# Optimization experiments

Hardware: AMD Instinct MI355X
Metric: run time of the kernel (lower is better)

Reference implementation:

```python
import jax, jax.numpy as jnp
import numpy as np

M, N = 4096, 4096


def _makhoul_perm(n):
    # Makhoul even/odd reordering: v[k] = x[2k] for k < ceil(n/2),
    # v[n-1-k] = x[2k+1] for the rest. This is the same input permutation
    # the dct2_fft2 kernel applies before its rfft2.
    idx = np.empty(n, dtype=np.int32)
    half = (n + 1) // 2
    idx[:half] = 2 * np.arange(half)
    idx[half:] = 2 * (n - 1 - np.arange(half, n)) + 1
    return jnp.asarray(idx)


def _dct2_1d_last(x):
    # Unnormalized DCT-II along the last axis via a same-length FFT plus
    # twiddle (expk) multiply:  C[k] = Re( exp(-i*pi*k/(2n)) * FFT(v)[k] )
    # which equals sum_m x[m] * cos(pi*k*(2m+1)/(2n)).
    n = x.shape[-1]
    v = jnp.take(x, _makhoul_perm(n), axis=-1)
    V = jnp.fft.fft(v, axis=-1)
    k = jnp.arange(n)
    expk = jnp.exp((-1j * np.pi / (2.0 * n)) * k)  # twiddle factors (expkM/expkN)
    return jnp.real(V * expk).astype(x.dtype)


def setup_inputs() -> dict:
    key = jax.random.key(0)
    x = jax.random.normal(key, (M, N), dtype=jnp.float32)
    return {"x": x}


def reference(x):
    # Separable 2D DCT-II: along axis -1 (uses expkN), then axis -2 (expkM).
    y = _dct2_1d_last(x)        # DCT over columns index (length N)
    y = _dct2_1d_last(y.T).T    # DCT over rows index (length M)
    return y
```

## Files before the change

### kernel.cpp

```cpp
#include <hip/hip_runtime.h>
#include <stdint.h>


#define NF 4096

__device__ __forceinline__ int physi(int e) { return e ^ ((e >> 4) & 15); }

__device__ __forceinline__ float2 cadd(float2 a, float2 b) {
    float2 r; r.x = a.x + b.x; r.y = a.y + b.y; return r;
}
__device__ __forceinline__ float2 csub(float2 a, float2 b) {
    float2 r; r.x = a.x - b.x; r.y = a.y - b.y; return r;
}
__device__ __forceinline__ float2 cmulc(float2 a, float2 b) {
    float2 r; r.x = a.x * b.x - a.y * b.y; r.y = a.x * b.y + a.y * b.x; return r;
}
__device__ __forceinline__ float2 rotm(float2 a) {
    float2 r; r.x = a.y; r.y = -a.x; return r;
}

__global__ __launch_bounds__(256) void setup_tables(float* __restrict__ tw,
                                                    float* __restrict__ ek) {
    int idx = blockIdx.x * 256 + threadIdx.x;
    if (idx < 4672) {
        int Ls, rel;
        if (idx < 64)       { Ls = 8;   rel = idx; }
        else if (idx < 576) { Ls = 64;  rel = idx - 64; }
        else                { Ls = 512; rel = idx - 576; }
        int p = rel >> 3, u = rel & 7;
        float phi = (float)(p * u) * (6.283185307179586f / (8.0f * (float)Ls));
        float s, c; __sincosf(phi, &s, &c);
        tw[2 * idx]     = c;
        tw[2 * idx + 1] = -s;
    } else if (idx < 8768) {
        int k = idx - 4672;
        float th = (float)k * (3.141592653589793f / 8192.0f);
        float s, c; __sincosf(th, &s, &c);
        ek[2 * k]     = c;
        ek[2 * k + 1] = s;
    }
}

#define RADIX8(x, E0, E1, E2, E3, O0, g1, g2, g3)                              \
    float2 t0 = cadd(x[0], x[4]), t1 = csub(x[0], x[4]);                       \
    float2 t2 = cadd(x[2], x[6]), t3 = csub(x[2], x[6]);                       \
    float2 E0 = cadd(t0, t2), E2 = csub(t0, t2);                               \
    float2 r3 = rotm(t3);                                                      \
    float2 E1 = cadd(t1, r3), E3 = csub(t1, r3);                               \
    float2 s0 = cadd(x[1], x[5]), s1 = csub(x[1], x[5]);                       \
    float2 s2 = cadd(x[3], x[7]), s3 = csub(x[3], x[7]);                       \
    float2 O0 = cadd(s0, s2), O2 = csub(s0, s2);                               \
    float2 r7 = rotm(s3);                                                      \
    float2 O1 = cadd(s1, r7), O3 = csub(s1, r7);                               \
    const float SQ = 0.7071067811865476f;                                      \
    float2 g1; g1.x = SQ * (O1.x + O1.y); g1.y = SQ * (O1.y - O1.x);           \
    float2 g2 = rotm(O2);                                                      \
    float2 g3; g3.x = SQ * (O3.y - O3.x); g3.y = -SQ * (O3.x + O3.y);

__global__ __launch_bounds__(512) void dct_rows(const float* __restrict__ In,
                                                float* __restrict__ Out,
                                                const float* __restrict__ tw,
                                                const float* __restrict__ ek) {
    __shared__ float2 buf[NF];
    const int j = threadIdx.x;
    const int b = blockIdx.x;
    const float* in0 = In + (size_t)(2 * b) * NF;
    const float* in1 = in0 + NF;
    float* out0 = Out + (size_t)b * NF;
    float* out1 = Out + (size_t)(4095 - b) * NF;

    float2 x[8];

    #pragma unroll
    for (int k = 0; k < 8; ++k) {
        int n = j + 512 * k;
        int idx = (n < 2048) ? (2 * n) : (8191 - 2 * n);
        x[k].x = in0[idx];
        x[k].y = in1[idx];
    }
    {
        RADIX8(x, E0, E1, E2, E3, O0, g1, g2, g3)
        int wb = 8 * j;
        buf[physi(wb)]     = cadd(E0, O0);
        buf[physi(wb + 1)] = cadd(E1, g1);
        buf[physi(wb + 2)] = cadd(E2, g2);
        buf[physi(wb + 3)] = cadd(E3, g3);
        buf[physi(wb + 4)] = csub(E0, O0);
        buf[physi(wb + 5)] = csub(E1, g1);
        buf[physi(wb + 6)] = csub(E2, g2);
        buf[physi(wb + 7)] = csub(E3, g3);
    }
    __syncthreads();

    #pragma unroll
    for (int t = 1; t < 3; ++t) {
        const int Ls = 1 << (3 * t);
        const int twoff = (t == 1) ? 0 : 64;
        const int p = j & (Ls - 1);
        const int q = j >> (3 * t);
        #pragma unroll
        for (int k = 0; k < 8; ++k)
            x[k] = buf[physi(j + 512 * k)];
        const float2* twp = (const float2*)tw + twoff + p * 8;
        #pragma unroll
        for (int k = 1; k < 8; ++k)
            x[k] = cmulc(x[k], twp[k]);
        RADIX8(x, E0, E1, E2, E3, O0, g1, g2, g3)
        __syncthreads();
        int wb = p + 8 * Ls * q;
        buf[physi(wb)]          = cadd(E0, O0);
        buf[physi(wb + Ls)]     = cadd(E1, g1);
        buf[physi(wb + 2 * Ls)] = cadd(E2, g2);
        buf[physi(wb + 3 * Ls)] = cadd(E3, g3);
        buf[physi(wb + 4 * Ls)] = csub(E0, O0);
        buf[physi(wb + 5 * Ls)] = csub(E1, g1);
        buf[physi(wb + 6 * Ls)] = csub(E2, g2);
        buf[physi(wb + 7 * Ls)] = csub(E3, g3);
        __syncthreads();
    }

    float2 o[8];
    {
        #pragma unroll
        for (int k = 0; k < 8; ++k)
            x[k] = buf[physi(j + 512 * k)];
        const float2* twp = (const float2*)tw + 576 + j * 8;
        #pragma unroll
        for (int k = 1; k < 8; ++k)
            x[k] = cmulc(x[k], twp[k]);
        RADIX8(x, E0, E1, E2, E3, O0, g1, g2, g3)
        o[0] = cadd(E0, O0); o[1] = cadd(E1, g1);
        o[2] = cadd(E2, g2); o[3] = cadd(E3, g3);
        o[4] = csub(E0, O0); o[5] = csub(E1, g1);
        o[6] = csub(E2, g2); o[7] = csub(E3, g3);
        #pragma unroll
        for (int r = 0; r < 8; ++r)
            buf[physi(j + 512 * r)] = o[r];
    }
    __syncthreads();

    #pragma unroll
    for (int i = 0; i < 8; ++i) {
        int k = j + 512 * i;
        int m = (NF - k) & (NF - 1);
        float2 Zk = o[i];
        float2 Zm = buf[physi(m)];
        float2 E = ((const float2*)ek)[k];
        out0[k] = 0.5f * ((Zk.x + Zm.x) * E.x + (Zk.y - Zm.y) * E.y);
        out1[k] = 0.5f * ((Zk.y + Zm.y) * E.x - (Zk.x - Zm.x) * E.y);
    }
}

__global__ __launch_bounds__(256) void col_fft1(const float* __restrict__ V,
                                                float* __restrict__ S,
                                                const float* __restrict__ tw) {
    __shared__ float2 T[64][32];
    const int ct = blockIdx.x, n1 = blockIdx.y;
    const int t = threadIdx.x;
    const int cp = t & 31, j = t >> 5;
    const float2* inb = (const float2*)V + (size_t)ct * 32 + cp;

    float2 x[8];
    #pragma unroll
    for (int k = 0; k < 8; ++k) {
        int row = n1 + 64 * (j + 8 * k);
        x[k] = inb[(size_t)row * 2048];
    }
    {
        RADIX8(x, E0, E1, E2, E3, O0, g1, g2, g3)
        T[8 * j + 0][cp] = cadd(E0, O0);
        T[8 * j + 1][cp] = cadd(E1, g1);
        T[8 * j + 2][cp] = cadd(E2, g2);
        T[8 * j + 3][cp] = cadd(E3, g3);
        T[8 * j + 4][cp] = csub(E0, O0);
        T[8 * j + 5][cp] = csub(E1, g1);
        T[8 * j + 6][cp] = csub(E2, g2);
        T[8 * j + 7][cp] = csub(E3, g3);
    }
    __syncthreads();

    float2 o[8];
    {
        #pragma unroll
        for (int k = 0; k < 8; ++k)
            x[k] = T[j + 8 * k][cp];
        const float2* twp = (const float2*)tw + j * 8;
        #pragma unroll
        for (int k = 1; k < 8; ++k)
            x[k] = cmulc(x[k], twp[k]);
        RADIX8(x, E0, E1, E2, E3, O0, g1, g2, g3)
        o[0] = cadd(E0, O0); o[1] = cadd(E1, g1);
        o[2] = cadd(E2, g2); o[3] = cadd(E3, g3);
        o[4] = csub(E0, O0); o[5] = csub(E1, g1);
        o[6] = csub(E2, g2); o[7] = csub(E3, g3);
    }

    float2* outb = (float2*)S + (size_t)ct * 32 + cp;
    #pragma unroll
    for (int i = 0; i < 8; ++i) {
        int k2 = j + 8 * i;
        float phi = (float)(n1 * k2) * -1.5339807878856412e-3f;
        float s, c; __sincosf(phi, &s, &c);
        float2 w; w.x = c; w.y = s;
        float2 h = cmulc(o[i], w);
        outb[(size_t)(64 * k2 + n1) * 2048] = h;
    }
}

__global__ __launch_bounds__(512) void col_fft2(const float* __restrict__ S,
                                                float* __restrict__ Out,
                                                const float* __restrict__ tw,
                                                const float* __restrict__ ek) {
    __shared__ float2 T[2][64][32];
    const int ct = blockIdx.x, bp = blockIdx.y;
    const int ga = bp, gb = (bp == 0) ? 32 : 64 - bp;
    const int t = threadIdx.x;
    const int cp = t & 31, j = (t >> 5) & 7, gi = t >> 8;
    const int g = gi ? gb : ga;
    const float2* inb = (const float2*)S + (size_t)ct * 32 + cp;

    float2 x[8];
    #pragma unroll
    for (int k = 0; k < 8; ++k)
        x[k] = inb[(size_t)(64 * g + j + 8 * k) * 2048];
    {
        RADIX8(x, E0, E1, E2, E3, O0, g1, g2, g3)
        T[gi][8 * j + 0][cp] = cadd(E0, O0);
        T[gi][8 * j + 1][cp] = cadd(E1, g1);
        T[gi][8 * j + 2][cp] = cadd(E2, g2);
        T[gi][8 * j + 3][cp] = cadd(E3, g3);
        T[gi][8 * j + 4][cp] = csub(E0, O0);
        T[gi][8 * j + 5][cp] = csub(E1, g1);
        T[gi][8 * j + 6][cp] = csub(E2, g2);
        T[gi][8 * j + 7][cp] = csub(E3, g3);
    }
    __syncthreads();

    float2 o[8];
    {
        #pragma unroll
        for (int k = 0; k < 8; ++k)
            x[k] = T[gi][j + 8 * k][cp];
        const float2* twp = (const float2*)tw + j * 8;
        #pragma unroll
        for (int k = 1; k < 8; ++k)
            x[k] = cmulc(x[k], twp[k]);
        RADIX8(x, E0, E1, E2, E3, O0, g1, g2, g3)
        o[0] = cadd(E0, O0); o[1] = cadd(E1, g1);
        o[2] = cadd(E2, g2); o[3] = cadd(E3, g3);
        o[4] = csub(E0, O0); o[5] = csub(E1, g1);
        o[6] = csub(E2, g2); o[7] = csub(E3, g3);
        #pragma unroll
        for (int i = 0; i < 8; ++i)
            T[gi][j + 8 * i][cp] = o[i];
    }
    __syncthreads();

    float2* outb = (float2*)Out + (size_t)ct * 32 + cp;
    #pragma unroll
    for (int i = 0; i < 8; ++i) {
        int k = 64 * (j + 8 * i) + g;
        int m = (NF - k) & (NF - 1);
        int gp = m & 63, k1p = m >> 6;
        float2 Zk = o[i];
        float2 Zm = T[(gp == ga) ? 0 : 1][k1p][cp];
        float2 E = ((const float2*)ek)[k];
        float2 r;
        r.x = 0.5f * ((Zk.x + Zm.x) * E.x + (Zk.y - Zm.y) * E.y);
        r.y = 0.5f * ((Zk.y + Zm.y) * E.x - (Zk.x - Zm.x) * E.y);
        outb[(size_t)k * 2048] = r;
    }
}

extern "C" void kernel_launch(void* const* d_in, const int* in_sizes, int n_in,
                              void* d_out, int out_size, void* d_ws, size_t ws_size,
                              hipStream_t stream) {
    const float* x = (const float*)d_in[0];
    float* out = (float*)d_out;

    float* tw = (float*)d_ws;
    float* ek = tw + 9344;
    float* B1 = ek + 8192;
    if (ws_size < (size_t)70144 + (size_t)NF * NF * sizeof(float)) return;

    setup_tables<<<35, 256, 0, stream>>>(tw, ek);
    dct_rows<<<NF / 2, 512, 0, stream>>>(x, out, tw, ek);
    col_fft1<<<dim3(64, 64), 256, 0, stream>>>(out, B1, tw);
    col_fft2<<<dim3(64, 32), 512, 0, stream>>>(B1, out, tw, ek);
}
```

Before: 169.6 us.

## Switch row FFT to radix-16 passes and cache column twiddles in shared memory

The 4096-point row FFT in dct_rows now uses three radix-16 passes with 256 threads, built on a new dft16 helper, instead of four radix-8 passes with 512 threads. This cuts shared-memory round trips and barriers, but raises register pressure per thread. The twiddle tables are rebuilt for radix-16 strides. col_fft1 now computes its 64 inter-stage twiddles once per block into shared memory rather than calling sincos per element.

After: 169.0 us. Within noise of the previous version (-0.3%).

```diff
diff --git a/kernel.cpp b/kernel.cpp
--- a/kernel.cpp
+++ b/kernel.cpp
@@ -22,18 +22,17 @@
 __global__ __launch_bounds__(256) void setup_tables(float* __restrict__ tw,
                                                     float* __restrict__ ek) {
     int idx = blockIdx.x * 256 + threadIdx.x;
-    if (idx < 4672) {
-        int Ls, rel;
-        if (idx < 64)       { Ls = 8;   rel = idx; }
-        else if (idx < 576) { Ls = 64;  rel = idx - 64; }
-        else                { Ls = 512; rel = idx - 576; }
-        int p = rel >> 3, u = rel & 7;
-        float phi = (float)(p * u) * (6.283185307179586f / (8.0f * (float)Ls));
+    if (idx < 4416) {
+        int p, u; float denom;
+        if (idx < 64)       { p = idx >> 3;         u = idx & 7;  denom = 64.0f; }
+        else if (idx < 320) { int r = idx - 64;  p = r >> 4; u = r & 15; denom = 256.0f; }
+        else                { int r = idx - 320; p = r >> 4; u = r & 15; denom = 4096.0f; }
+        float phi = (float)(p * u) * (6.283185307179586f / denom);
         float s, c; __sincosf(phi, &s, &c);
         tw[2 * idx]     = c;
         tw[2 * idx + 1] = -s;
-    } else if (idx < 8768) {
-        int k = idx - 4672;
+    } else if (idx < 8512) {
+        int k = idx - 4416;
         float th = (float)k * (3.141592653589793f / 8192.0f);
         float s, c; __sincosf(th, &s, &c);
         ek[2 * k]     = c;
@@ -41,14 +40,14 @@
     }
 }
 
-#define RADIX8(x, E0, E1, E2, E3, O0, g1, g2, g3)                              \
-    float2 t0 = cadd(x[0], x[4]), t1 = csub(x[0], x[4]);                       \
-    float2 t2 = cadd(x[2], x[6]), t3 = csub(x[2], x[6]);                       \
+#define RADIX8(Xv, E0, E1, E2, E3, O0, g1, g2, g3)                             \
+    float2 t0 = cadd(Xv[0], Xv[4]), t1 = csub(Xv[0], Xv[4]);                   \
+    float2 t2 = cadd(Xv[2], Xv[6]), t3 = csub(Xv[2], Xv[6]);                   \
     float2 E0 = cadd(t0, t2), E2 = csub(t0, t2);                               \
     float2 r3 = rotm(t3);                                                      \
     float2 E1 = cadd(t1, r3), E3 = csub(t1, r3);                               \
-    float2 s0 = cadd(x[1], x[5]), s1 = csub(x[1], x[5]);                       \
-    float2 s2 = cadd(x[3], x[7]), s3 = csub(x[3], x[7]);                       \
+    float2 s0 = cadd(Xv[1], Xv[5]), s1 = csub(Xv[1], Xv[5]);                   \
+    float2 s2 = cadd(Xv[3], Xv[7]), s3 = csub(Xv[3], Xv[7]);                   \
     float2 O0 = cadd(s0, s2), O2 = csub(s0, s2);                               \
     float2 r7 = rotm(s3);                                                      \
     float2 O1 = cadd(s1, r7), O3 = csub(s1, r7);                               \
@@ -57,7 +56,46 @@
     float2 g2 = rotm(O2);                                                      \
     float2 g3; g3.x = SQ * (O3.y - O3.x); g3.y = -SQ * (O3.x + O3.y);
 
-__global__ __launch_bounds__(512) void dct_rows(const float* __restrict__ In,
+__device__ __forceinline__ void dft16(float2* x) {
+    float2 E[8], O[8];
+    {
+        float2 a[8];
+        #pragma unroll
+        for (int m = 0; m < 8; ++m) a[m] = x[2 * m];
+        RADIX8(a, E0, E1, E2, E3, O0, g1, g2, g3)
+        E[0] = cadd(E0, O0); E[1] = cadd(E1, g1);
+        E[2] = cadd(E2, g2); E[3] = cadd(E3, g3);
+        E[4] = csub(E0, O0); E[5] = csub(E1, g1);
+        E[6] = csub(E2, g2); E[7] = csub(E3, g3);
+    }
+    {
+        float2 a[8];
+        #pragma unroll
+        for (int m = 0; m < 8; ++m) a[m] = x[2 * m + 1];
+        RADIX8(a, E0, E1, E2, E3, O0, g1, g2, g3)
+        O[0] = cadd(E0, O0); O[1] = cadd(E1, g1);
+        O[2] = cadd(E2, g2); O[3] = cadd(E3, g3);
+        O[4] = csub(E0, O0); O[5] = csub(E1, g1);
+        O[6] = csub(E2, g2); O[7] = csub(E3, g3);
+    }
+    const float2 W1 = { 0.9238795325112867f, -0.3826834323650898f};
+    const float2 W2 = { 0.7071067811865476f, -0.7071067811865476f};
+    const float2 W3 = { 0.3826834323650898f, -0.9238795325112867f};
+    const float2 W5 = {-0.3826834323650898f, -0.9238795325112867f};
+    const float2 W6 = {-0.7071067811865476f, -0.7071067811865476f};
+    const float2 W7 = {-0.9238795325112867f, -0.3826834323650898f};
+    float2 t;
+    x[0] = cadd(E[0], O[0]);  x[8]  = csub(E[0], O[0]);
+    t = cmulc(O[1], W1); x[1] = cadd(E[1], t); x[9]  = csub(E[1], t);
+    t = cmulc(O[2], W2); x[2] = cadd(E[2], t); x[10] = csub(E[2], t);
+    t = cmulc(O[3], W3); x[3] = cadd(E[3], t); x[11] = csub(E[3], t);
+    t = rotm(O[4]);      x[4] = cadd(E[4], t); x[12] = csub(E[4], t);
+    t = cmulc(O[5], W5); x[5] = cadd(E[5], t); x[13] = csub(E[5], t);
+    t = cmulc(O[6], W6); x[6] = cadd(E[6], t); x[14] = csub(E[6], t);
+    t = cmulc(O[7], W7); x[7] = cadd(E[7], t); x[15] = csub(E[7], t);
+}
+
+__global__ __launch_bounds__(256) void dct_rows(const float* __restrict__ In,
                                                 float* __restrict__ Out,
                                                 const float* __restrict__ tw,
                                                 const float* __restrict__ ek) {
@@ -69,81 +107,59 @@
     float* out0 = Out + (size_t)b * NF;
     float* out1 = Out + (size_t)(4095 - b) * NF;
 
-    float2 x[8];
-
-    #pragma unroll
-    for (int k = 0; k < 8; ++k) {
-        int n = j + 512 * k;
+    float2 x[16];
+
+    #pragma unroll
+    for (int k = 0; k < 16; ++k) {
+        int n = j + 256 * k;
         int idx = (n < 2048) ? (2 * n) : (8191 - 2 * n);
         x[k].x = in0[idx];
         x[k].y = in1[idx];
     }
-    {
-        RADIX8(x, E0, E1, E2, E3, O0, g1, g2, g3)
-        int wb = 8 * j;
-        buf[physi(wb)]     = cadd(E0, O0);
-        buf[physi(wb + 1)] = cadd(E1, g1);
-        buf[physi(wb + 2)] = cadd(E2, g2);
-        buf[physi(wb + 3)] = cadd(E3, g3);
-        buf[physi(wb + 4)] = csub(E0, O0);
-        buf[physi(wb + 5)] = csub(E1, g1);
-        buf[physi(wb + 6)] = csub(E2, g2);
-        buf[physi(wb + 7)] = csub(E3, g3);
-    }
-    __syncthreads();
-
-    #pragma unroll
-    for (int t = 1; t < 3; ++t) {
-        const int Ls = 1 << (3 * t);
-        const int twoff = (t == 1) ? 0 : 64;
-        const int p = j & (Ls - 1);
-        const int q = j >> (3 * t);
-        #pragma unroll
-        for (int k = 0; k < 8; ++k)
-            x[k] = buf[physi(j + 512 * k)];
-        const float2* twp = (const float2*)tw + twoff + p * 8;
-        #pragma unroll
-        for (int k = 1; k < 8; ++k)
+    dft16(x);
+    #pragma unroll
+    for (int i = 0; i < 16; ++i)
+        buf[physi(16 * j + i)] = x[i];
+    __syncthreads();
+
+    {
+        const int p = j & 15, q = j >> 4;
+        #pragma unroll
+        for (int k = 0; k < 16; ++k)
+            x[k] = buf[physi(j + 256 * k)];
+        const float2* twp = (const float2*)tw + 64 + p * 16;
+        #pragma unroll
+        for (int k = 1; k < 16; ++k)
             x[k] = cmulc(x[k], twp[k]);
-        RADIX8(x, E0, E1, E2, E3, O0, g1, g2, g3)
+        dft16(x);
         __syncthreads();
-        int wb = p + 8 * Ls * q;
-        buf[physi(wb)]          = cadd(E0, O0);
-        buf[physi(wb + Ls)]     = cadd(E1, g1);
-        buf[physi(wb + 2 * Ls)] = cadd(E2, g2);
-        buf[physi(wb + 3 * Ls)] = cadd(E3, g3);
-        buf[physi(wb + 4 * Ls)] = csub(E0, O0);
-        buf[physi(wb + 5 * Ls)] = csub(E1, g1);
-        buf[physi(wb + 6 * Ls)] = csub(E2, g2);
-        buf[physi(wb + 7 * Ls)] = csub(E3, g3);
+        int wb = p + 256 * q;
+        #pragma unroll
+        for (int i = 0; i < 16; ++i)
+            buf[physi(wb + 16 * i)] = x[i];
         __syncthreads();
     }
 
-    float2 o[8];
-    {
-        #pragma unroll
-        for (int k = 0; k < 8; ++k)
-            x[k] = buf[physi(j + 512 * k)];
-        const float2* twp = (const float2*)tw + 576 + j * 8;
-        #pragma unroll
-        for (int k = 1; k < 8; ++k)
+    {
+        #pragma unroll
+        for (int k = 0; k < 16; ++k)
+            x[k] = buf[physi(j + 256 * k)];
+        const float2* twp = (const float2*)tw + 320 + j * 16;
+        #pragma unroll
+        for (int k = 1; k < 16; ++k)
             x[k] = cmulc(x[k], twp[k]);
-        RADIX8(x, E0, E1, E2, E3, O0, g1, g2, g3)
-        o[0] = cadd(E0, O0); o[1] = cadd(E1, g1);
-        o[2] = cadd(E2, g2); o[3] = cadd(E3, g3);
-        o[4] = csub(E0, O0); o[5] = csub(E1, g1);
-        o[6] = csub(E2, g2); o[7] = csub(E3, g3);
-        #pragma unroll
-        for (int r = 0; r < 8; ++r)
-            buf[physi(j + 512 * r)] = o[r];
-    }
-    __syncthreads();
-
-    #pragma unroll
-    for (int i = 0; i < 8; ++i) {
-        int k = j + 512 * i;
+        dft16(x);
+        #pragma unroll
+        for (int i = 0; i < 16; ++i)
+            buf[physi(j + 256 * i)] = x[i];
+    }
+    __syncthreads();
+
+    #pragma unroll
+    for (int i = 0; i < 16; ++i) {
+        int k = j + 256 * i;
         int m = (NF - k) & (NF - 1);
-        float2 Zk = o[i];
+        float2 Zk = x[i];
         float2 Zm = buf[physi(m)];
         float2 E = ((const float2*)ek)[k];
         out0[k] = 0.5f * ((Zk.x + Zm.x) * E.x + (Zk.y - Zm.y) * E.y);
@@ -155,10 +171,19 @@
                                                 float* __restrict__ S,
                                                 const float* __restrict__ tw) {
     __shared__ float2 T[64][32];
+    __shared__ float2 w64[64];
     const int ct = blockIdx.x, n1 = blockIdx.y;
     const int t = threadIdx.x;
     const int cp = t & 31, j = t >> 5;
     const float2* inb = (const float2*)V + (size_t)ct * 32 + cp;
+
+    if (t < 64) {
+        int m = (n1 * t) & 4095;
+        float phi = (float)m * -1.5339807878856412e-3f;
+        float s, c; __sincosf(phi, &s, &c);
+        float2 w; w.x = c; w.y = s;
+        w64[t] = w;
+    }
 
     float2 x[8];
     #pragma unroll
@@ -199,10 +224,7 @@
     #pragma unroll
     for (int i = 0; i < 8; ++i) {
         int k2 = j + 8 * i;
-        float phi = (float)(n1 * k2) * -1.5339807878856412e-3f;
-        float s, c; __sincosf(phi, &s, &c);
-        float2 w; w.x = c; w.y = s;
-        float2 h = cmulc(o[i], w);
+        float2 h = cmulc(o[i], w64[k2]);
         outb[(size_t)(64 * k2 + n1) * 2048] = h;
     }
 }
@@ -279,12 +301,12 @@
     float* out = (float*)d_out;
 
     float* tw = (float*)d_ws;
-    float* ek = tw + 9344;
+    float* ek = tw + 8832;
     float* B1 = ek + 8192;
-    if (ws_size < (size_t)70144 + (size_t)NF * NF * sizeof(float)) return;
-
-    setup_tables<<<35, 256, 0, stream>>>(tw, ek);
-    dct_rows<<<NF / 2, 512, 0, stream>>>(x, out, tw, ek);
+    if (ws_size < (size_t)68096 + (size_t)NF * NF * sizeof(float)) return;
+
+    setup_tables<<<34, 256, 0, stream>>>(tw, ek);
+    dct_rows<<<NF / 2, 256, 0, stream>>>(x, out, tw, ek);
     col_fft1<<<dim3(64, 64), 256, 0, stream>>>(out, B1, tw);
     col_fft2<<<dim3(64, 32), 512, 0, stream>>>(B1, out, tw, ek);
 }
```
